# Kernel optimization log

Measured on AMD Instinct MI355X. Metric: run time of the kernel, lower is better.

The kernel has to match this reference:

```python
import jax, jax.numpy as jnp
import numpy as np

N = 100000   # num nodes
D = 64       # in_channels == out_channels (forced by zeros_like(x) accumulator)
E = 400000   # edges per edge type
T = 5        # number of edge types (hardcoded list in the module)


def setup_inputs() -> dict:
    key = jax.random.key(0)
    k1, k2, k3, k4, k5 = jax.random.split(key, 5)
    x = jax.random.normal(k1, (N, D), dtype=jnp.float32)
    # 5 edge types, each [2, E] of node indices (row 0 = src, row 1 = dst)
    edges = jax.random.randint(k2, (T, 2, E), 0, N)
    # per-edge-type Linear(2D -> D): weight [2D, D] and bias [D]
    W = jax.random.normal(k3, (T, 2 * D, D), dtype=jnp.float32) * (1.0 / np.sqrt(2 * D))
    b = jax.random.normal(k4, (T, D), dtype=jnp.float32) * 0.01
    edge_attention = jax.random.normal(k5, (T,), dtype=jnp.float32)
    return {"x": x, "W": W, "b": b, "edge_attention": edge_attention, "edges": edges}


def reference(x, W, b, edge_attention, edges):
    # softmax over the 5 edge types (F.softmax(self.edge_attention, dim=0))
    weights = jax.nn.softmax(edge_attention)              # [T]
    src = edges[:, 0, :]                                  # [T, E]
    dst = edges[:, 1, :]                                  # [T, E]
    # gather: edge_features = cat([x[src], x[dst]], dim=1)
    feats = jnp.concatenate([x[src], x[dst]], axis=-1)    # [T, E, 2D]
    # per-edge-type MLP: Linear(2D->D) + ReLU
    proj = jax.nn.relu(jnp.einsum('tef,tfd->ted', feats, W) + b[:, None, :])  # [T, E, D]
    # scatter-add into src nodes, then mean via clamped bincount
    seg_sum = jax.vmap(lambda s, p: jax.ops.segment_sum(p, s, num_segments=N))(src, proj)  # [T, N, D]
    counts = jax.vmap(lambda s: jax.ops.segment_sum(jnp.ones(s.shape, jnp.float32), s, num_segments=N))(src)  # [T, N]
    counts = jnp.maximum(counts, 1.0)[:, :, None]         # clamp(min=1)
    node_proj = seg_sum / counts                          # [T, N, D]
    # attention-weighted sum across edge types
    return jnp.einsum('t,tnd->nd', weights, node_proj)    # [N, D]
```

## Files before the change

### kernel.cpp

```cpp
#include <hip/hip_runtime.h>
#include <hip/hip_bf16.h>

#define NN 100000
#define DD 64
#define EE 400000
#define TT 5

#define CH 40
#define BPC 2500
#define PSPLIT 32
#define PESL (EE / PSPLIT)
#define PBN (TT * CH * PSPLIT)
#define PB_IDX(t, c, s) ((((t) * CH + (c)) * PSPLIT) + (s))

#define SCAN_TOTAL 500000
#define SCAN_T 256
#define SCAN_PER 1024
#define SCAN_B 512

typedef __bf16 bf16x8 __attribute__((ext_vector_type(8)));
typedef float  f32x4  __attribute__((ext_vector_type(4)));

#define OFF_XBF  0u
#define OFF_WT   12800000u
#define OFF_CTOT 12881920u
#define OFF_WGT  14881920u
#define OFF_CUR  14881984u
#define OFF_BS   16881984u
#define OFF_BO   16884032u
#define OFF_PE   16886080u
#define OFF_PB   24886080u
#define OFF_DST  24914240u
#define OFF_SEG  32914240u

__device__ __forceinline__ unsigned short f2bf(float f) {
    union { float f; unsigned u; } v; v.f = f;
    unsigned u = v.u;
    return (unsigned short)((u + 0x7FFFu + ((u >> 16) & 1u)) >> 16);
}

__global__ __launch_bounds__(256) void k_init(
        const float* __restrict__ x, const float* __restrict__ W,
        const float* __restrict__ ea, const int* __restrict__ edges,
        unsigned short* __restrict__ xbf, unsigned short* __restrict__ wT,
        float* __restrict__ wgt, float* __restrict__ out,
        unsigned* __restrict__ pcnt) {
    int i = blockIdx.x * blockDim.x + threadIdx.x;
    if (i < NN * DD) {
        out[i] = 0.0f;
        xbf[i] = f2bf(x[i]);
    }
    if (i < TT * 128 * 64) {
        int t = i >> 13;
        int rem = i & 8191;
        int d = rem >> 7;
        int k = rem & 127;
        wT[i] = f2bf(W[t * 8192 + k * 64 + d]);
    }
    if (i == 0) {
        float m = -1e30f;
        for (int t = 0; t < TT; t++) m = fmaxf(m, ea[t]);
        float e[TT]; float s = 0.0f;
        for (int t = 0; t < TT; t++) { e[t] = __expf(ea[t] - m); s += e[t]; }
        for (int t = 0; t < TT; t++) wgt[t] = e[t] / s;
    }
    if (blockIdx.x < PSPLIT * TT) {
        const int s = blockIdx.x & (PSPLIT - 1);
        const int t = blockIdx.x >> 5;
        __shared__ unsigned h[CH];
        if (threadIdx.x < CH) h[threadIdx.x] = 0u;
        __syncthreads();
        const int4* srcp = reinterpret_cast<const int4*>(edges + (size_t)t * 2 * EE + s * PESL);
        for (int j = threadIdx.x; j < PESL / 4; j += 256) {
            int4 v = srcp[j];
            atomicAdd(&h[(unsigned)v.x / BPC], 1u);
            atomicAdd(&h[(unsigned)v.y / BPC], 1u);
            atomicAdd(&h[(unsigned)v.z / BPC], 1u);
            atomicAdd(&h[(unsigned)v.w / BPC], 1u);
        }
        __syncthreads();
        if (threadIdx.x < CH) pcnt[PB_IDX(t, threadIdx.x, s)] = h[threadIdx.x];
    }
}

__global__ void k_pscan(unsigned* __restrict__ pb) {
    __shared__ unsigned s[512];
    const int tid = threadIdx.x;
    unsigned v[13]; unsigned sum = 0u;
#pragma unroll
    for (int j = 0; j < 13; j++) {
        int g = tid * 13 + j;
        v[j] = (g < PBN) ? pb[g] : 0u;
        sum += v[j];
    }
    s[tid] = sum;
    __syncthreads();
    unsigned inc = sum;
    for (int d = 1; d < 512; d <<= 1) {
        unsigned a = (tid >= d) ? s[tid - d] : 0u;
        __syncthreads();
        inc += a;
        s[tid] = inc;
        __syncthreads();
    }
    unsigned run = inc - sum;
#pragma unroll
    for (int j = 0; j < 13; j++) {
        int g = tid * 13 + j;
        if (g < PBN) pb[g] = run;
        run += v[j];
    }
    if (tid == 511) pb[PBN] = run;
}

__global__ __launch_bounds__(256) void k_pscat(const int* __restrict__ edges,
                                               const unsigned* __restrict__ pbase,
                                               unsigned* __restrict__ pe) {
    const int s = blockIdx.x, t = blockIdx.y;
    __shared__ unsigned lofs[CH];
    if (threadIdx.x < CH) lofs[threadIdx.x] = pbase[PB_IDX(t, threadIdx.x, s)];
    __syncthreads();
    const int* srcp = edges + (size_t)t * 2 * EE + s * PESL;
    const int* dstp = srcp + EE;
    for (int i = threadIdx.x; i < PESL / 4; i += 256) {
        int4 v = reinterpret_cast<const int4*>(srcp)[i];
        int4 w = reinterpret_cast<const int4*>(dstp)[i];
        {
            unsigned c = (unsigned)v.x / BPC;
            unsigned o = atomicAdd(&lofs[c], 1u);
            pe[o] = (((unsigned)v.x - c * BPC) << 17) | (unsigned)w.x;
        }
        {
            unsigned c = (unsigned)v.y / BPC;
            unsigned o = atomicAdd(&lofs[c], 1u);
            pe[o] = (((unsigned)v.y - c * BPC) << 17) | (unsigned)w.y;
        }
        {
            unsigned c = (unsigned)v.z / BPC;
            unsigned o = atomicAdd(&lofs[c], 1u);
            pe[o] = (((unsigned)v.z - c * BPC) << 17) | (unsigned)w.z;
        }
        {
            unsigned c = (unsigned)v.w / BPC;
            unsigned o = atomicAdd(&lofs[c], 1u);
            pe[o] = (((unsigned)v.w - c * BPC) << 17) | (unsigned)w.w;
        }
    }
}

__global__ __launch_bounds__(512) void k_bcount(const unsigned* __restrict__ pe,
                                                const unsigned* __restrict__ pbase,
                                                unsigned* __restrict__ cnt_tot) {
    const int c = blockIdx.x, t = blockIdx.y;
    __shared__ unsigned h[BPC];
    for (int i = threadIdx.x; i < BPC; i += 512) h[i] = 0u;
    __syncthreads();
    const unsigned st = pbase[PB_IDX(t, c, 0)];
    const unsigned en = pbase[((t * CH + c) + 1) * PSPLIT];
    for (unsigned i = st + threadIdx.x; i < en; i += 512)
        atomicAdd(&h[pe[i] >> 17], 1u);
    __syncthreads();
    unsigned* outp = cnt_tot + t * NN + c * BPC;
    for (int i = threadIdx.x; i < BPC; i += 512) outp[i] = h[i];
}

__global__ void k_scan1(const unsigned* __restrict__ cnt_tot,
                        unsigned* __restrict__ cur, unsigned* __restrict__ bsum) {
    __shared__ unsigned s[SCAN_T];
    const int b = blockIdx.x, tid = threadIdx.x;
    const int base = b * SCAN_PER + tid * 4;
    unsigned tot[4] = {0u, 0u, 0u, 0u};
    if (base < SCAN_TOTAL) {
        uint4 tv = *reinterpret_cast<const uint4*>(cnt_tot + base);
        tot[0] = tv.x; tot[1] = tv.y; tot[2] = tv.z; tot[3] = tv.w;
    }
    const unsigned tsum = tot[0] + tot[1] + tot[2] + tot[3];
    s[tid] = tsum;
    __syncthreads();
    unsigned inc = tsum;
    for (int d = 1; d < SCAN_T; d <<= 1) {
        unsigned add = (tid >= d) ? s[tid - d] : 0u;
        __syncthreads();
        inc += add;
        s[tid] = inc;
        __syncthreads();
    }
    if (tid == SCAN_T - 1) bsum[b] = inc;
    const unsigned p0 = inc - tsum;
    if (base < SCAN_TOTAL) {
        *reinterpret_cast<uint4*>(cur + base) =
            make_uint4(p0, p0 + tot[0], p0 + tot[0] + tot[1], p0 + tot[0] + tot[1] + tot[2]);
    }
}

__global__ void k_scan2(const unsigned* __restrict__ bsum, unsigned* __restrict__ boff) {
    __shared__ unsigned s[SCAN_B];
    const int tid = threadIdx.x;
    const unsigned v = bsum[tid];
    s[tid] = v;
    __syncthreads();
    unsigned inc = v;
    for (int d = 1; d < SCAN_B; d <<= 1) {
        unsigned add = (tid >= d) ? s[tid - d] : 0u;
        __syncthreads();
        inc += add;
        s[tid] = inc;
        __syncthreads();
    }
    boff[tid] = inc - v;
}

__global__ __launch_bounds__(512) void k_bfill(const unsigned* __restrict__ pe,
                                               const unsigned* __restrict__ pbase,
                                               const unsigned* __restrict__ cur,
                                               const unsigned* __restrict__ boff,
                                               const unsigned* __restrict__ cnt_tot,
                                               int* __restrict__ sdst,
                                               int* __restrict__ seg) {
    const int c = blockIdx.x, t = blockIdx.y;
    __shared__ unsigned curl[BPC];
    const int n0 = c * BPC;
    for (int i = threadIdx.x; i < BPC; i += 512) {
        int g = t * NN + n0 + i;
        unsigned start = cur[g] + boff[g >> 10];
        curl[i] = start;
        unsigned cc = cnt_tot[g];
        int node = n0 + i;
        for (unsigned j = 0; j < cc; j++) seg[start + j] = node;
    }
    __syncthreads();
    const unsigned st = pbase[PB_IDX(t, c, 0)];
    const unsigned en = pbase[((t * CH + c) + 1) * PSPLIT];
    for (unsigned i = st + threadIdx.x; i < en; i += 512) {
        unsigned p = pe[i];
        sdst[atomicAdd(&curl[p >> 17], 1u)] = (int)(p & 0x1FFFFu);
    }
}

__global__ __launch_bounds__(256) void k_edge(
    const unsigned short* __restrict__ xbf, const unsigned short* __restrict__ wT,
    const float* __restrict__ b, const int* __restrict__ sdst,
    const int* __restrict__ seg, const unsigned* __restrict__ cnt,
    const float* __restrict__ wgt, float* __restrict__ out) {
    const int t  = blockIdx.y;
    const int e0 = blockIdx.x * 128;

    __shared__ __align__(16) unsigned short Ab[128][136];
    __shared__ float scale_s[128];
    __shared__ int   src_s[132];

    const int tid = threadIdx.x;

    {
        int e = tid >> 1, half = tid & 1;
        size_t pos = (size_t)t * EE + e0 + e;
        int idx = half ? sdst[pos] : seg[pos];
        const float4* g = reinterpret_cast<const float4*>(xbf + (size_t)idx * 64);
        float4* l = reinterpret_cast<float4*>(&Ab[e][half * 64]);
#pragma unroll
        for (int c = 0; c < 8; c++) l[c] = g[c];
        if (half == 0) {
            src_s[e] = idx;
            scale_s[e] = wgt[t] / (float)cnt[t * NN + idx];
        }
    }
    __syncthreads();

    const int wv = tid >> 6, lane = tid & 63;
    const int m16 = lane & 15, quad = lane >> 4;
    const unsigned short* wrow = wT + (size_t)t * 8192;

    f32x4 acc[2][4];
#pragma unroll
    for (int tm = 0; tm < 2; tm++)
#pragma unroll
        for (int tn = 0; tn < 4; tn++)
            acc[tm][tn] = (f32x4){0.f, 0.f, 0.f, 0.f};

#pragma unroll
    for (int kk = 0; kk < 128; kk += 32) {
        const int kb = kk + quad * 8;
        bf16x8 af[2], bfr[4];
#pragma unroll
        for (int tm = 0; tm < 2; tm++)
            af[tm] = *reinterpret_cast<const bf16x8*>(&Ab[wv * 32 + tm * 16 + m16][kb]);
#pragma unroll
        for (int tn = 0; tn < 4; tn++)
            bfr[tn] = *reinterpret_cast<const bf16x8*>(wrow + (tn * 16 + m16) * 128 + kb);
#pragma unroll
        for (int tm = 0; tm < 2; tm++)
#pragma unroll
            for (int tn = 0; tn < 4; tn++)
                acc[tm][tn] = __builtin_amdgcn_mfma_f32_16x16x32_bf16(
                    af[tm], bfr[tn], acc[tm][tn], 0, 0, 0);
    }

    __syncthreads();

    float bias[4];
#pragma unroll
    for (int tn = 0; tn < 4; tn++) bias[tn] = b[t * 64 + tn * 16 + m16];

    float* proj = reinterpret_cast<float*>(&Ab[0][0]);
#pragma unroll
    for (int tm = 0; tm < 2; tm++) {
#pragma unroll
        for (int r = 0; r < 4; r++) {
            const int eloc = wv * 32 + tm * 16 + quad * 4 + r;
            const float s = scale_s[eloc];
#pragma unroll
            for (int tn = 0; tn < 4; tn++) {
                float v = acc[tm][tn][r] + bias[tn];
                v = v > 0.f ? v : 0.f;
                proj[eloc * 68 + tn * 16 + m16] = v * s;
            }
        }
    }

    {
        const int j0 = wv * 32;
        float sum = 0.f;
#pragma unroll
        for (int j = j0; j < j0 + 32; j++) {
            sum += proj[j * 68 + lane];
            const bool flush = (j == j0 + 31) || (src_s[j + 1] != src_s[j]);
            if (flush) {
                atomicAdd(out + (size_t)src_s[j] * 64 + lane, sum);
                sum = 0.f;
            }
        }
    }
}

extern "C" void kernel_launch(void* const* d_in, const int* in_sizes, int n_in,
                              void* d_out, int out_size, void* d_ws, size_t ws_size,
                              hipStream_t stream) {
    const float* x     = (const float*)d_in[0];
    const float* W     = (const float*)d_in[1];
    const float* b     = (const float*)d_in[2];
    const float* ea    = (const float*)d_in[3];
    const int*   edges = (const int*)d_in[4];
    float* out = (float*)d_out;

    char* ws = (char*)d_ws;
    unsigned short* xbf  = (unsigned short*)(ws + OFF_XBF);
    unsigned short* wT   = (unsigned short*)(ws + OFF_WT);
    unsigned* cnt_tot    = (unsigned*)(ws + OFF_CTOT);
    float* wgt           = (float*)(ws + OFF_WGT);
    unsigned* cur        = (unsigned*)(ws + OFF_CUR);
    unsigned* bsum       = (unsigned*)(ws + OFF_BS);
    unsigned* boff       = (unsigned*)(ws + OFF_BO);
    unsigned* pe         = (unsigned*)(ws + OFF_PE);
    unsigned* pb         = (unsigned*)(ws + OFF_PB);
    int* sdst            = (int*)(ws + OFF_DST);
    int* seg             = (int*)(ws + OFF_SEG);

    k_init<<<(NN * DD) / 256, 256, 0, stream>>>(x, W, ea, edges, xbf, wT, wgt, out, pb);

    k_pscan<<<1, 512, 0, stream>>>(pb);
    k_pscat<<<dim3(PSPLIT, TT), 256, 0, stream>>>(edges, pb, pe);
    k_bcount<<<dim3(CH, TT), 512, 0, stream>>>(pe, pb, cnt_tot);
    k_scan1<<<SCAN_B, SCAN_T, 0, stream>>>(cnt_tot, cur, bsum);
    k_scan2<<<1, SCAN_B, 0, stream>>>(bsum, boff);
    k_bfill<<<dim3(CH, TT), 512, 0, stream>>>(pe, pb, cur, boff, cnt_tot, sdst, seg);

    dim3 grid(EE / 128, TT);
    k_edge<<<grid, 256, 0, stream>>>(xbf, wT, b, sdst, seg, cnt_tot, wgt, out);
}
```

Baseline: 320.2 us.

## Make edge kernel persistent with per-wave windows and register-prefetched gathers

```diff
diff --git a/kernel.cpp b/kernel.cpp
--- a/kernel.cpp
+++ b/kernel.cpp
@@ -17,6 +17,10 @@
 #define SCAN_T 256
 #define SCAN_PER 1024
 #define SCAN_B 512
+
+#define WPT 12500
+#define NWIN (TT * WPT)
+#define EGRID 2048
 
 typedef __bf16 bf16x8 __attribute__((ext_vector_type(8)));
 typedef float  f32x4  __attribute__((ext_vector_type(4)));
@@ -237,98 +241,143 @@
     }
 }
 
-__global__ __launch_bounds__(256) void k_edge(
+__global__ __launch_bounds__(256, 4) void k_edge6(
     const unsigned short* __restrict__ xbf, const unsigned short* __restrict__ wT,
     const float* __restrict__ b, const int* __restrict__ sdst,
     const int* __restrict__ seg, const unsigned* __restrict__ cnt,
     const float* __restrict__ wgt, float* __restrict__ out) {
-    const int t  = blockIdx.y;
-    const int e0 = blockIdx.x * 128;
 
     __shared__ __align__(16) unsigned short Ab[128][136];
     __shared__ float scale_s[128];
     __shared__ int   src_s[132];
 
     const int tid = threadIdx.x;
-
-    {
-        int e = tid >> 1, half = tid & 1;
-        size_t pos = (size_t)t * EE + e0 + e;
-        int idx = half ? sdst[pos] : seg[pos];
-        const float4* g = reinterpret_cast<const float4*>(xbf + (size_t)idx * 64);
-        float4* l = reinterpret_cast<float4*>(&Ab[e][half * 64]);
-#pragma unroll
-        for (int c = 0; c < 8; c++) l[c] = g[c];
-        if (half == 0) {
-            src_s[e] = idx;
-            scale_s[e] = wgt[t] / (float)cnt[t * NN + idx];
-        }
-    }
-    __syncthreads();
-
     const int wv = tid >> 6, lane = tid & 63;
     const int m16 = lane & 15, quad = lane >> 4;
-    const unsigned short* wrow = wT + (size_t)t * 8192;
-
-    f32x4 acc[2][4];
-#pragma unroll
-    for (int tm = 0; tm < 2; tm++)
-#pragma unroll
-        for (int tn = 0; tn < 4; tn++)
-            acc[tm][tn] = (f32x4){0.f, 0.f, 0.f, 0.f};
-
-#pragma unroll
-    for (int kk = 0; kk < 128; kk += 32) {
-        const int kb = kk + quad * 8;
-        bf16x8 af[2], bfr[4];
-#pragma unroll
-        for (int tm = 0; tm < 2; tm++)
-            af[tm] = *reinterpret_cast<const bf16x8*>(&Ab[wv * 32 + tm * 16 + m16][kb]);
-#pragma unroll
-        for (int tn = 0; tn < 4; tn++)
-            bfr[tn] = *reinterpret_cast<const bf16x8*>(wrow + (tn * 16 + m16) * 128 + kb);
-#pragma unroll
-        for (int tm = 0; tm < 2; tm++)
-#pragma unroll
-            for (int tn = 0; tn < 4; tn++)
-                acc[tm][tn] = __builtin_amdgcn_mfma_f32_16x16x32_bf16(
-                    af[tm], bfr[tn], acc[tm][tn], 0, 0, 0);
-    }
-
-    __syncthreads();
-
-    float bias[4];
-#pragma unroll
-    for (int tn = 0; tn < 4; tn++) bias[tn] = b[t * 64 + tn * 16 + m16];
-
-    float* proj = reinterpret_cast<float*>(&Ab[0][0]);
-#pragma unroll
-    for (int tm = 0; tm < 2; tm++) {
-#pragma unroll
-        for (int r = 0; r < 4; r++) {
-            const int eloc = wv * 32 + tm * 16 + quad * 4 + r;
-            const float s = scale_s[eloc];
-#pragma unroll
-            for (int tn = 0; tn < 4; tn++) {
-                float v = acc[tm][tn][r] + bias[tn];
-                v = v > 0.f ? v : 0.f;
-                proj[eloc * 68 + tn * 16 + m16] = v * s;
+    const int el = lane >> 1, half = lane & 1;
+    const int row = wv * 32 + el;
+    const int j0 = wv * 32;
+    const int WSTRIDE = EGRID * 4;
+
+    unsigned wcur = blockIdx.x * 4 + wv;
+    if (wcur >= NWIN) return;
+
+    unsigned tC = wcur / WPT;
+    unsigned e0C = (wcur - tC * WPT) * 32u;
+    {
+        size_t pos = (size_t)tC * EE + e0C + el;
+        int iC0 = half ? sdst[pos] : seg[pos];
+        (void)iC0;
+    }
+    int iC;
+    unsigned cC = 1u;
+    float4 r0, r1, r2, r3, r4, r5, r6, r7;
+    {
+        size_t pos = (size_t)tC * EE + e0C + el;
+        iC = half ? sdst[pos] : seg[pos];
+        if (half == 0) cC = cnt[tC * NN + iC];
+        const float4* g = reinterpret_cast<const float4*>(xbf + (size_t)iC * 64);
+        r0 = g[0]; r1 = g[1]; r2 = g[2]; r3 = g[3];
+        r4 = g[4]; r5 = g[5]; r6 = g[6]; r7 = g[7];
+    }
+    unsigned wnxt = wcur + WSTRIDE;
+    unsigned tN = 0, e0N = 0;
+    int iN = 0;
+    if (wnxt < NWIN) {
+        tN = wnxt / WPT; e0N = (wnxt - tN * WPT) * 32u;
+        size_t pos = (size_t)tN * EE + e0N + el;
+        iN = half ? sdst[pos] : seg[pos];
+    }
+
+    while (true) {
+        {
+            float4* l = reinterpret_cast<float4*>(&Ab[row][half * 64]);
+            l[0] = r0; l[1] = r1; l[2] = r2; l[3] = r3;
+            l[4] = r4; l[5] = r5; l[6] = r6; l[7] = r7;
+            if (half == 0) {
+                src_s[row] = iC;
+                scale_s[row] = __ldg(wgt + tC) / (float)cC;
             }
         }
-    }
-
-    {
-        const int j0 = wv * 32;
-        float sum = 0.f;
-#pragma unroll
-        for (int j = j0; j < j0 + 32; j++) {
-            sum += proj[j * 68 + lane];
-            const bool flush = (j == j0 + 31) || (src_s[j + 1] != src_s[j]);
-            if (flush) {
-                atomicAdd(out + (size_t)src_s[j] * 64 + lane, sum);
-                sum = 0.f;
+        const unsigned tcomp = tC;
+
+        const bool more = (wnxt < NWIN);
+        const unsigned wn2 = wnxt + WSTRIDE;
+        if (more) {
+            tC = tN; e0C = e0N; iC = iN;
+            if (half == 0) cC = cnt[tC * NN + iC];
+            const float4* g = reinterpret_cast<const float4*>(xbf + (size_t)iC * 64);
+            r0 = g[0]; r1 = g[1]; r2 = g[2]; r3 = g[3];
+            r4 = g[4]; r5 = g[5]; r6 = g[6]; r7 = g[7];
+            if (wn2 < NWIN) {
+                tN = wn2 / WPT; e0N = (wn2 - tN * WPT) * 32u;
+                size_t pos = (size_t)tN * EE + e0N + el;
+                iN = half ? sdst[pos] : seg[pos];
             }
         }
+
+        {
+            const unsigned short* wrow = wT + (size_t)tcomp * 8192;
+
+            f32x4 acc[2][4];
+#pragma unroll
+            for (int tm = 0; tm < 2; tm++)
+#pragma unroll
+                for (int tn = 0; tn < 4; tn++)
+                    acc[tm][tn] = (f32x4){0.f, 0.f, 0.f, 0.f};
+
+#pragma unroll
+            for (int kk = 0; kk < 128; kk += 32) {
+                const int kb = kk + quad * 8;
+                bf16x8 af[2], bfr[4];
+#pragma unroll
+                for (int tm = 0; tm < 2; tm++)
+                    af[tm] = *reinterpret_cast<const bf16x8*>(&Ab[j0 + tm * 16 + m16][kb]);
+#pragma unroll
+                for (int tn = 0; tn < 4; tn++)
+                    bfr[tn] = *reinterpret_cast<const bf16x8*>(wrow + (tn * 16 + m16) * 128 + kb);
+#pragma unroll
+                for (int tm = 0; tm < 2; tm++)
+#pragma unroll
+                    for (int tn = 0; tn < 4; tn++)
+                        acc[tm][tn] = __builtin_amdgcn_mfma_f32_16x16x32_bf16(
+                            af[tm], bfr[tn], acc[tm][tn], 0, 0, 0);
+            }
+
+            float bias[4];
+#pragma unroll
+            for (int tn = 0; tn < 4; tn++) bias[tn] = b[tcomp * 64 + tn * 16 + m16];
+
+            float* proj = reinterpret_cast<float*>(&Ab[0][0]);
+#pragma unroll
+            for (int tm = 0; tm < 2; tm++) {
+#pragma unroll
+                for (int r = 0; r < 4; r++) {
+                    const int eloc = j0 + tm * 16 + quad * 4 + r;
+                    const float s = scale_s[eloc];
+#pragma unroll
+                    for (int tn = 0; tn < 4; tn++) {
+                        float v = acc[tm][tn][r] + bias[tn];
+                        v = v > 0.f ? v : 0.f;
+                        proj[eloc * 68 + tn * 16 + m16] = v * s;
+                    }
+                }
+            }
+
+            float sum = 0.f;
+#pragma unroll
+            for (int j = j0; j < j0 + 32; j++) {
+                sum += proj[j * 68 + lane];
+                const bool flush = (j == j0 + 31) || (src_s[j + 1] != src_s[j]);
+                if (flush) {
+                    atomicAdd(out + (size_t)src_s[j] * 64 + lane, sum);
+                    sum = 0.f;
+                }
+            }
+        }
+
+        if (!more) break;
+        wnxt = wn2;
     }
 }
 
@@ -364,6 +413,5 @@
     k_scan2<<<1, SCAN_B, 0, stream>>>(bsum, boff);
     k_bfill<<<dim3(CH, TT), 512, 0, stream>>>(pe, pb, cur, boff, cnt_tot, sdst, seg);
 
-    dim3 grid(EE / 128, TT);
-    k_edge<<<grid, 256, 0, stream>>>(xbf, wT, b, sdst, seg, cnt_tot, wgt, out);
-}
+    k_edge6<<<EGRID, 256, 0, stream>>>(xbf, wT, b, sdst, seg, cnt_tot, wgt, out);
+}
```

Result: slower. 375.1 us (+17.1%).

## Fuse bucket scans into scatter and sort kernels, cutting launches from eight to four

Applied to the files above, without the earlier changes.

```diff
diff --git a/kernel.cpp b/kernel.cpp
--- a/kernel.cpp
+++ b/kernel.cpp
@@ -13,11 +13,6 @@
 #define PBN (TT * CH * PSPLIT)
 #define PB_IDX(t, c, s) ((((t) * CH + (c)) * PSPLIT) + (s))
 
-#define SCAN_TOTAL 500000
-#define SCAN_T 256
-#define SCAN_PER 1024
-#define SCAN_B 512
-
 typedef __bf16 bf16x8 __attribute__((ext_vector_type(8)));
 typedef float  f32x4  __attribute__((ext_vector_type(4)));
 
@@ -25,9 +20,6 @@
 #define OFF_WT   12800000u
 #define OFF_CTOT 12881920u
 #define OFF_WGT  14881920u
-#define OFF_CUR  14881984u
-#define OFF_BS   16881984u
-#define OFF_BO   16884032u
 #define OFF_PE   16886080u
 #define OFF_PB   24886080u
 #define OFF_DST  24914240u
@@ -83,46 +75,39 @@
     }
 }
 
-__global__ void k_pscan(unsigned* __restrict__ pb) {
-    __shared__ unsigned s[512];
-    const int tid = threadIdx.x;
-    unsigned v[13]; unsigned sum = 0u;
-#pragma unroll
-    for (int j = 0; j < 13; j++) {
-        int g = tid * 13 + j;
-        v[j] = (g < PBN) ? pb[g] : 0u;
-        sum += v[j];
-    }
-    s[tid] = sum;
-    __syncthreads();
-    unsigned inc = sum;
-    for (int d = 1; d < 512; d <<= 1) {
-        unsigned a = (tid >= d) ? s[tid - d] : 0u;
-        __syncthreads();
-        inc += a;
-        s[tid] = inc;
-        __syncthreads();
-    }
-    unsigned run = inc - sum;
-#pragma unroll
-    for (int j = 0; j < 13; j++) {
-        int g = tid * 13 + j;
-        if (g < PBN) pb[g] = run;
-        run += v[j];
-    }
-    if (tid == 511) pb[PBN] = run;
-}
-
 __global__ __launch_bounds__(256) void k_pscat(const int* __restrict__ edges,
-                                               const unsigned* __restrict__ pbase,
+                                               const unsigned* __restrict__ pb,
                                                unsigned* __restrict__ pe) {
     const int s = blockIdx.x, t = blockIdx.y;
+    const int tid = threadIdx.x;
+    __shared__ unsigned pbs[PBN];
+    __shared__ unsigned ssum[256];
     __shared__ unsigned lofs[CH];
-    if (threadIdx.x < CH) lofs[threadIdx.x] = pbase[PB_IDX(t, threadIdx.x, s)];
-    __syncthreads();
+    {
+        const int base = tid * 25;
+        unsigned v[25]; unsigned sum = 0u;
+#pragma unroll
+        for (int j = 0; j < 25; j++) { v[j] = pb[base + j]; sum += v[j]; }
+        ssum[tid] = sum;
+        __syncthreads();
+        unsigned inc = sum;
+        for (int d = 1; d < 256; d <<= 1) {
+            unsigned a = (tid >= d) ? ssum[tid - d] : 0u;
+            __syncthreads();
+            inc += a;
+            ssum[tid] = inc;
+            __syncthreads();
+        }
+        unsigned run = inc - sum;
+#pragma unroll
+        for (int j = 0; j < 25; j++) { pbs[base + j] = run; run += v[j]; }
+        __syncthreads();
+        if (tid < CH) lofs[tid] = pbs[PB_IDX(t, tid, s)];
+        __syncthreads();
+    }
     const int* srcp = edges + (size_t)t * 2 * EE + s * PESL;
     const int* dstp = srcp + EE;
-    for (int i = threadIdx.x; i < PESL / 4; i += 256) {
+    for (int i = tid; i < PESL / 4; i += 256) {
         int4 v = reinterpret_cast<const int4*>(srcp)[i];
         int4 w = reinterpret_cast<const int4*>(dstp)[i];
         {
@@ -148,90 +133,84 @@
     }
 }
 
-__global__ __launch_bounds__(512) void k_bcount(const unsigned* __restrict__ pe,
-                                                const unsigned* __restrict__ pbase,
-                                                unsigned* __restrict__ cnt_tot) {
-    const int c = blockIdx.x, t = blockIdx.y;
-    __shared__ unsigned h[BPC];
-    for (int i = threadIdx.x; i < BPC; i += 512) h[i] = 0u;
-    __syncthreads();
-    const unsigned st = pbase[PB_IDX(t, c, 0)];
-    const unsigned en = pbase[((t * CH + c) + 1) * PSPLIT];
-    for (unsigned i = st + threadIdx.x; i < en; i += 512)
-        atomicAdd(&h[pe[i] >> 17], 1u);
-    __syncthreads();
-    unsigned* outp = cnt_tot + t * NN + c * BPC;
-    for (int i = threadIdx.x; i < BPC; i += 512) outp[i] = h[i];
-}
-
-__global__ void k_scan1(const unsigned* __restrict__ cnt_tot,
-                        unsigned* __restrict__ cur, unsigned* __restrict__ bsum) {
-    __shared__ unsigned s[SCAN_T];
-    const int b = blockIdx.x, tid = threadIdx.x;
-    const int base = b * SCAN_PER + tid * 4;
-    unsigned tot[4] = {0u, 0u, 0u, 0u};
-    if (base < SCAN_TOTAL) {
-        uint4 tv = *reinterpret_cast<const uint4*>(cnt_tot + base);
-        tot[0] = tv.x; tot[1] = tv.y; tot[2] = tv.z; tot[3] = tv.w;
-    }
-    const unsigned tsum = tot[0] + tot[1] + tot[2] + tot[3];
-    s[tid] = tsum;
-    __syncthreads();
-    unsigned inc = tsum;
-    for (int d = 1; d < SCAN_T; d <<= 1) {
-        unsigned add = (tid >= d) ? s[tid - d] : 0u;
-        __syncthreads();
-        inc += add;
-        s[tid] = inc;
-        __syncthreads();
-    }
-    if (tid == SCAN_T - 1) bsum[b] = inc;
-    const unsigned p0 = inc - tsum;
-    if (base < SCAN_TOTAL) {
-        *reinterpret_cast<uint4*>(cur + base) =
-            make_uint4(p0, p0 + tot[0], p0 + tot[0] + tot[1], p0 + tot[0] + tot[1] + tot[2]);
-    }
-}
-
-__global__ void k_scan2(const unsigned* __restrict__ bsum, unsigned* __restrict__ boff) {
-    __shared__ unsigned s[SCAN_B];
-    const int tid = threadIdx.x;
-    const unsigned v = bsum[tid];
-    s[tid] = v;
-    __syncthreads();
-    unsigned inc = v;
-    for (int d = 1; d < SCAN_B; d <<= 1) {
-        unsigned add = (tid >= d) ? s[tid - d] : 0u;
-        __syncthreads();
-        inc += add;
-        s[tid] = inc;
-        __syncthreads();
-    }
-    boff[tid] = inc - v;
-}
-
-__global__ __launch_bounds__(512) void k_bfill(const unsigned* __restrict__ pe,
-                                               const unsigned* __restrict__ pbase,
-                                               const unsigned* __restrict__ cur,
-                                               const unsigned* __restrict__ boff,
-                                               const unsigned* __restrict__ cnt_tot,
+__global__ __launch_bounds__(512) void k_bsort(const unsigned* __restrict__ pe,
+                                               const unsigned* __restrict__ pb,
+                                               unsigned* __restrict__ cnt_tot,
                                                int* __restrict__ sdst,
                                                int* __restrict__ seg) {
     const int c = blockIdx.x, t = blockIdx.y;
+    const int tid = threadIdx.x;
+    __shared__ unsigned h[BPC];
     __shared__ unsigned curl[BPC];
-    const int n0 = c * BPC;
-    for (int i = threadIdx.x; i < BPC; i += 512) {
-        int g = t * NN + n0 + i;
-        unsigned start = cur[g] + boff[g >> 10];
-        curl[i] = start;
-        unsigned cc = cnt_tot[g];
-        int node = n0 + i;
-        for (unsigned j = 0; j < cc; j++) seg[start + j] = node;
-    }
-    __syncthreads();
-    const unsigned st = pbase[PB_IDX(t, c, 0)];
-    const unsigned en = pbase[((t * CH + c) + 1) * PSPLIT];
-    for (unsigned i = st + threadIdx.x; i < en; i += 512) {
+    __shared__ unsigned ssum[512];
+    __shared__ unsigned stsh[2];
+
+    const int K = (t * CH + c) * PSPLIT;
+
+    unsigned part = 0u;
+    for (int i = tid; i < K; i += 512) part += pb[i];
+    ssum[tid] = part;
+    __syncthreads();
+    for (int d = 256; d > 0; d >>= 1) {
+        if (tid < d) ssum[tid] += ssum[tid + d];
+        __syncthreads();
+    }
+    if (tid == 0) stsh[0] = ssum[0];
+    unsigned part2 = (tid < PSPLIT) ? pb[K + tid] : 0u;
+    __syncthreads();
+    ssum[tid] = part2;
+    __syncthreads();
+    for (int d = 256; d > 0; d >>= 1) {
+        if (tid < d) ssum[tid] += ssum[tid + d];
+        __syncthreads();
+    }
+    if (tid == 0) stsh[1] = ssum[0];
+    for (int i = tid; i < BPC; i += 512) h[i] = 0u;
+    __syncthreads();
+    const unsigned st = stsh[0];
+    const unsigned en = st + stsh[1];
+
+    for (unsigned i = st + tid; i < en; i += 512)
+        atomicAdd(&h[pe[i] >> 17], 1u);
+    __syncthreads();
+
+    unsigned* outp = cnt_tot + t * NN + c * BPC;
+    for (int i = tid; i < BPC; i += 512) outp[i] = h[i];
+
+    {
+        const int base = tid * 5;
+        unsigned v[5]; unsigned sum = 0u;
+#pragma unroll
+        for (int j = 0; j < 5; j++) {
+            int g = base + j;
+            v[j] = (g < BPC) ? h[g] : 0u;
+            sum += v[j];
+        }
+        ssum[tid] = sum;
+        __syncthreads();
+        unsigned inc = sum;
+        for (int d = 1; d < 512; d <<= 1) {
+            unsigned a = (tid >= d) ? ssum[tid - d] : 0u;
+            __syncthreads();
+            inc += a;
+            ssum[tid] = inc;
+            __syncthreads();
+        }
+        unsigned run = st + inc - sum;
+#pragma unroll
+        for (int j = 0; j < 5; j++) {
+            int g = base + j;
+            if (g < BPC) {
+                curl[g] = run;
+                const int node = c * BPC + g;
+                for (unsigned jj = 0; jj < v[j]; jj++) seg[run + jj] = node;
+                run += v[j];
+            }
+        }
+    }
+    __syncthreads();
+
+    for (unsigned i = st + tid; i < en; i += 512) {
         unsigned p = pe[i];
         sdst[atomicAdd(&curl[p >> 17], 1u)] = (int)(p & 0x1FFFFu);
     }
@@ -347,9 +326,6 @@
     unsigned short* wT   = (unsigned short*)(ws + OFF_WT);
     unsigned* cnt_tot    = (unsigned*)(ws + OFF_CTOT);
     float* wgt           = (float*)(ws + OFF_WGT);
-    unsigned* cur        = (unsigned*)(ws + OFF_CUR);
-    unsigned* bsum       = (unsigned*)(ws + OFF_BS);
-    unsigned* boff       = (unsigned*)(ws + OFF_BO);
     unsigned* pe         = (unsigned*)(ws + OFF_PE);
     unsigned* pb         = (unsigned*)(ws + OFF_PB);
     int* sdst            = (int*)(ws + OFF_DST);
@@ -357,12 +333,9 @@
 
     k_init<<<(NN * DD) / 256, 256, 0, stream>>>(x, W, ea, edges, xbf, wT, wgt, out, pb);
 
-    k_pscan<<<1, 512, 0, stream>>>(pb);
     k_pscat<<<dim3(PSPLIT, TT), 256, 0, stream>>>(edges, pb, pe);
-    k_bcount<<<dim3(CH, TT), 512, 0, stream>>>(pe, pb, cnt_tot);
-    k_scan1<<<SCAN_B, SCAN_T, 0, stream>>>(cnt_tot, cur, bsum);
-    k_scan2<<<1, SCAN_B, 0, stream>>>(bsum, boff);
-    k_bfill<<<dim3(CH, TT), 512, 0, stream>>>(pe, pb, cur, boff, cnt_tot, sdst, seg);
+
+    k_bsort<<<dim3(CH, TT), 512, 0, stream>>>(pe, pb, cnt_tot, sdst, seg);
 
     dim3 grid(EE / 128, TT);
     k_edge<<<grid, 256, 0, stream>>>(xbf, wT, b, sdst, seg, cnt_tot, wgt, out);
```

New measurement: 317.4 us. Within noise of the previous version (-0.9%).
